# Optimization experiments

Measured on AMD Instinct MI355X. Metric: run time of the kernel, lower is better.

The kernel has to match this reference:

```python
import jax, jax.numpy as jnp
import numpy as np

DIM = 768
HEADS = 12
HEAD_DIM = DIM // HEADS
SCALE = HEAD_DIM ** -0.5
EPS = 1e-6


def setup_inputs() -> dict:
    key = jax.random.key(0)
    ks = jax.random.split(key, 10)
    B, Nq, Nk, C = 4, 4096, 4096, DIM
    std = C ** -0.5
    return {
        "x_q": jax.random.normal(ks[0], (B, Nq, C), jnp.float32),
        "x_kv": jax.random.normal(ks[1], (B, Nk, C), jnp.float32),
        "Wq": jax.random.normal(ks[2], (C, C), jnp.float32) * std,
        "bq": jnp.zeros((C,), jnp.float32),
        "Wk": jax.random.normal(ks[3], (C, C), jnp.float32) * std,
        "bk": jnp.zeros((C,), jnp.float32),
        "Wv": jax.random.normal(ks[4], (C, C), jnp.float32) * std,
        "bv": jnp.zeros((C,), jnp.float32),
        "Wp": jax.random.normal(ks[5], (C, C), jnp.float32) * std,
        "bp": jnp.zeros((C,), jnp.float32),
    }


def _phi(x):
    # ELU(alpha=1) + 1 positive feature map
    return jax.nn.elu(x) + 1.0


def reference(x_q, x_kv, Wq, bq, Wk, bk, Wv, bv, Wp, bp):
    B, Nq, C = x_q.shape
    Nk = x_kv.shape[1]
    h, d = HEADS, HEAD_DIM
    # projections (torch Linear: x @ W.T + b)
    q = x_q @ Wq.T + bq   # [B,Nq,C]
    k = x_kv @ Wk.T + bk  # [B,Nk,C]
    v = x_kv @ Wv.T + bv  # [B,Nk,C]
    # split heads -> [B,h,N,d]
    q = q.reshape(B, Nq, h, d).transpose(0, 2, 1, 3) * SCALE
    k = k.reshape(B, Nk, h, d).transpose(0, 2, 1, 3)
    v = v.reshape(B, Nk, h, d).transpose(0, 2, 1, 3)
    q_phi = _phi(q)
    k_phi = _phi(k)
    # KV state [B,h,d,d] and normalizer sum [B,h,d]
    kv = jnp.einsum('bhnd,bhne->bhde', k_phi, v)
    k_sum = k_phi.sum(axis=2)
    out = jnp.einsum('bhnd,bhde->bhne', q_phi, kv)
    z = jnp.einsum('bhnd,bhd->bhn', q_phi, k_sum)[..., None] + EPS
    out = out / z
    out = out.transpose(0, 2, 1, 3).reshape(B, Nq, C)
    return out @ Wp.T + bp
```

## Files before the change

kernel.cpp:

```cpp
#include <hip/hip_runtime.h>
#include <hip/hip_bf16.h>
#include <cstdint>
#include <cstddef>

#define HD_B   4
#define SEQ    4096
#define CDIM   768
#define HEADS  12
#define HDIM   64
#define MROWS  (HD_B * SEQ)
#define QSCALE 0.125f
#define EPSV   1e-6f

typedef __attribute__((ext_vector_type(8))) short  short8v;
typedef __attribute__((ext_vector_type(4))) float  f32x4;

__device__ __forceinline__ unsigned short f2b(float f) {
    unsigned int u = __float_as_uint(f);
    u += 0x7FFFu + ((u >> 16) & 1u);
    return (unsigned short)(u >> 16);
}
__device__ __forceinline__ float b2f(unsigned short b) {
    return __uint_as_float(((unsigned int)b) << 16);
}
__device__ __forceinline__ float phi_f(float x) {
    return x > 0.f ? x + 1.f : __expf(x);
}

#define GLOAD_LDS16(g, l)                                             \
    __builtin_amdgcn_global_load_lds(                                 \
        (__attribute__((address_space(1))) void*)(void*)(g),          \
        (__attribute__((address_space(3))) void*)(l), 16, 0, 0)

__global__ void wcvt_all(const float* __restrict__ wq, const float* __restrict__ wk,
                         const float* __restrict__ wv, const float* __restrict__ wp,
                         unsigned short* __restrict__ dst) {
    const int y = blockIdx.y;
    const float* src = (y == 0) ? wq : (y == 1) ? wk : (y == 2) ? wv : wp;
    const int i = blockIdx.x * 256 + threadIdx.x;
    float4 v = reinterpret_cast<const float4*>(src)[i];
    ushort4 o;
    o.x = f2b(v.x); o.y = f2b(v.y); o.z = f2b(v.z); o.w = f2b(v.w);
    reinterpret_cast<ushort4*>(dst + (size_t)y * (CDIM * CDIM))[i] = o;
}

template <int KIND>
__global__ __launch_bounds__(256) void gemm_pipe(
    const float* __restrict__ Aq,
    const float* __restrict__ Akv,
    const unsigned short* __restrict__ Abf,
    const unsigned short* __restrict__ Wb,
    const float* __restrict__ b0,
    const float* __restrict__ b1,
    const float* __restrict__ b2,
    unsigned short* __restrict__ out_q,
    unsigned short* __restrict__ out_k,
    unsigned short* __restrict__ out_v,
    float* __restrict__ out_f)
{
    constexpr int K  = CDIM;
    constexpr int NC = (KIND == 0) ? 18 : 6;
    constexpr int T  = NC * 128;
    constexpr int NT = K / 64;

    __shared__ __align__(16) char smem[65536];

    const int tid  = threadIdx.x;
    const int lane = tid & 63;
    const int w    = tid >> 6;
    const int wr   = w >> 1, wc = w & 1;

    const int bid  = blockIdx.x;
    const int s    = (bid & 7) * (T >> 3) + (bid >> 3);
    const int colp = s % NC;
    const int rowp = s / NC;
    const int brow = rowp * 128;
    const int mode = (KIND == 0) ? (colp / 6) : 3;
    const int bcol = (KIND == 0) ? (colp % 6) * 128 : colp * 128;

    const float* A32 = (KIND == 0) ? (mode == 0 ? Aq : Akv) : nullptr;
    const unsigned short* Bp = Wb + ((KIND == 0) ? (size_t)mode * (K * K) : 0);

    const int r8  = lane >> 3;
    const int c8  = ((lane & 7) ^ r8) << 3;
    const int ar  = lane >> 4;
    const int ac  = (lane & 15) << 2;
    const int fr  = lane & 15;
    const int hi4 = lane >> 4;

    f32x4 acc[4][4];
#pragma unroll
    for (int i = 0; i < 4; ++i)
#pragma unroll
        for (int j = 0; j < 4; ++j)
            acc[i][j] = (f32x4){0.f, 0.f, 0.f, 0.f};

    auto stageB = [&](int buf, int k0) {
        char* dst = smem + 32768 + buf * 16384;
#pragma unroll
        for (int g = 0; g < 4; ++g) {
            const unsigned short* src =
                Bp + (size_t)(bcol + w * 32 + g * 8 + r8) * K + k0 + c8;
            GLOAD_LDS16(src, dst + (w * 32 + g * 8) * 128);
        }
    };
    auto stageA16 = [&](int buf, int k0) {
        char* dst = smem + buf * 16384;
#pragma unroll
        for (int g = 0; g < 4; ++g) {
            const unsigned short* src =
                Abf + (size_t)(brow + w * 32 + g * 8 + r8) * K + k0 + c8;
            GLOAD_LDS16(src, dst + (w * 32 + g * 8) * 128);
        }
    };
    auto loadA32 = [&](int k0, float4* f) {
#pragma unroll
        for (int j = 0; j < 8; ++j) {
            const int row = w * 32 + j * 4 + ar;
            f[j] = *(const float4*)(A32 + (size_t)(brow + row) * K + k0 + ac);
        }
    };
    auto writeA32 = [&](int buf, const float4* f) {
        char* dst = smem + buf * 16384;
#pragma unroll
        for (int j = 0; j < 8; ++j) {
            const int row = w * 32 + j * 4 + ar;
            unsigned int p0, p1;
            asm("v_cvt_pk_bf16_f32 %0, %1, %2" : "=v"(p0) : "v"(f[j].x), "v"(f[j].y));
            asm("v_cvt_pk_bf16_f32 %0, %1, %2" : "=v"(p1) : "v"(f[j].z), "v"(f[j].w));
            uint2 pk; pk.x = p0; pk.y = p1;
            *(uint2*)(dst + row * 128 + ((ac << 1) ^ ((row & 7) << 4))) = pk;
        }
    };
    auto compute = [&](int buf) {
        const char* Ab = smem + buf * 16384;
        const char* Bb = smem + 32768 + buf * 16384;
        short8v a[4][2];
#pragma unroll
        for (int i = 0; i < 4; ++i) {
            const int row = wr * 64 + i * 16 + fr;
#pragma unroll
            for (int ks = 0; ks < 2; ++ks)
                a[i][ks] = *(const short8v*)(Ab + row * 128 +
                              ((((ks << 2) + hi4) ^ (row & 7)) << 4));
        }
#pragma unroll
        for (int j = 0; j < 4; ++j) {
            const int row = wc * 64 + j * 16 + fr;
            short8v bb0 = *(const short8v*)(Bb + row * 128 + ((hi4 ^ (row & 7)) << 4));
            short8v bb1 = *(const short8v*)(Bb + row * 128 + (((4 + hi4) ^ (row & 7)) << 4));
#pragma unroll
            for (int i = 0; i < 4; ++i) {
                acc[i][j] = __builtin_amdgcn_mfma_f32_16x16x32_bf16(a[i][0], bb0, acc[i][j], 0, 0, 0);
                acc[i][j] = __builtin_amdgcn_mfma_f32_16x16x32_bf16(a[i][1], bb1, acc[i][j], 0, 0, 0);
            }
        }
    };

    if (KIND == 0) {
        float4 fA[8];
        stageB(0, 0);
        loadA32(0, fA);
        asm volatile("s_waitcnt vmcnt(0)" ::: "memory");
        writeA32(0, fA);
        __syncthreads();
        for (int t = 0; t < NT; ++t) {
            const int cur = t & 1, nxt = cur ^ 1;
            if (t < NT - 1) { stageB(nxt, (t + 1) * 64); loadA32((t + 1) * 64, fA); }
            __builtin_amdgcn_sched_barrier(0);
            compute(cur);
            if (t < NT - 1) {
                asm volatile("s_waitcnt vmcnt(0)" ::: "memory");
                writeA32(nxt, fA);
                __syncthreads();
            }
        }
    } else {
        stageB(0, 0);
        stageA16(0, 0);
        __syncthreads();
        for (int t = 0; t < NT; ++t) {
            const int cur = t & 1, nxt = cur ^ 1;
            if (t < NT - 1) { stageB(nxt, (t + 1) * 64); stageA16(nxt, (t + 1) * 64); }
            __builtin_amdgcn_sched_barrier(0);
            compute(cur);
            if (t < NT - 1) __syncthreads();
        }
    }
    __syncthreads();

    float* ep = (float*)(void*)smem + w * (16 * 68);
    const int rr = lane >> 2;
    const int cb = (lane & 3) * 4;
    const float* bptr = (KIND == 1) ? b0 : (mode == 0 ? b0 : (mode == 1 ? b1 : b2));
    unsigned short* o16 = (KIND == 0)
        ? (mode == 0 ? out_q : (mode == 1 ? out_k : out_v)) : nullptr;

    float4 bb[4];
#pragma unroll
    for (int q = 0; q < 4; ++q)
        bb[q] = *(const float4*)&bptr[bcol + wc * 64 + q * 16 + cb];

#pragma unroll
    for (int i = 0; i < 4; ++i) {
#pragma unroll
        for (int j = 0; j < 4; ++j)
#pragma unroll
            for (int r = 0; r < 4; ++r)
                ep[(hi4 * 4 + r) * 68 + j * 16 + fr] = acc[i][j][r];
#pragma unroll
        for (int q = 0; q < 4; ++q) {
            const int cc = q * 16 + cb;
            f32x4 v = *(const f32x4*)&ep[rr * 68 + cc];
            const int rg = brow + wr * 64 + i * 16 + rr;
            const int cg = bcol + wc * 64 + cc;
            const float4 bq = bb[q];
            if (KIND == 1) {
                float4 ov;
                ov.x = v[0] + bq.x; ov.y = v[1] + bq.y;
                ov.z = v[2] + bq.z; ov.w = v[3] + bq.w;
                *(float4*)(out_f + (size_t)rg * 768 + cg) = ov;
            } else {
                ushort4 ov;
                if (mode == 0) {
                    ov.x = f2b(phi_f((v[0] + bq.x) * QSCALE));
                    ov.y = f2b(phi_f((v[1] + bq.y) * QSCALE));
                    ov.z = f2b(phi_f((v[2] + bq.z) * QSCALE));
                    ov.w = f2b(phi_f((v[3] + bq.w) * QSCALE));
                } else if (mode == 1) {
                    ov.x = f2b(phi_f(v[0] + bq.x));
                    ov.y = f2b(phi_f(v[1] + bq.y));
                    ov.z = f2b(phi_f(v[2] + bq.z));
                    ov.w = f2b(phi_f(v[3] + bq.w));
                } else {
                    ov.x = f2b(v[0] + bq.x);
                    ov.y = f2b(v[1] + bq.y);
                    ov.z = f2b(v[2] + bq.z);
                    ov.w = f2b(v[3] + bq.w);
                }
                *(ushort4*)(o16 + (size_t)rg * 768 + cg) = ov;
            }
        }
    }
}

#define KVCH   128
#define KVITER 2
#define NCHUNK 16

__global__ __launch_bounds__(256) void kv_part(
    const unsigned short* __restrict__ kphi,
    const unsigned short* __restrict__ vmat,
    float* __restrict__ part)
{
    const int bh = blockIdx.y;
    const int b  = bh / HEADS, h = bh % HEADS;
    const int c  = blockIdx.x;
    __shared__ float Kl[KVCH][HDIM];
    __shared__ float Vl[KVCH][HDIM];
    const int t  = threadIdx.x;
    const int i  = t >> 2;
    const int jb = t & 3;

    float acc[16];
#pragma unroll
    for (int jj = 0; jj < 16; ++jj) acc[jj] = 0.f;
    float ksum = 0.f;

    for (int it = 0; it < KVITER; ++it) {
        const size_t rbase = (size_t)b * SEQ + (size_t)c * (KVCH * KVITER) + it * KVCH;
        __syncthreads();
        for (int l = 0; l < KVCH / 32; ++l) {
            int row = l * 32 + (t >> 3);
            int col = (t & 7) << 3;
            const size_t g = (rbase + row) * CDIM + h * HDIM + col;
            int4 kk = *(const int4*)(kphi + g);
            int4 vv = *(const int4*)(vmat + g);
            const unsigned short* kp = (const unsigned short*)&kk;
            const unsigned short* vp = (const unsigned short*)&vv;
#pragma unroll
            for (int q = 0; q < 8; ++q) {
                Kl[row][col + q] = b2f(kp[q]);
                Vl[row][col + q] = b2f(vp[q]);
            }
        }
        __syncthreads();
        for (int n = 0; n < KVCH; ++n) {
            float kf = Kl[n][i];
            const float4* vr = (const float4*)&Vl[n][jb * 16];
            float4 v0 = vr[0], v1 = vr[1], v2 = vr[2], v3 = vr[3];
            acc[0]  += kf * v0.x; acc[1]  += kf * v0.y; acc[2]  += kf * v0.z; acc[3]  += kf * v0.w;
            acc[4]  += kf * v1.x; acc[5]  += kf * v1.y; acc[6]  += kf * v1.z; acc[7]  += kf * v1.w;
            acc[8]  += kf * v2.x; acc[9]  += kf * v2.y; acc[10] += kf * v2.z; acc[11] += kf * v2.w;
            acc[12] += kf * v3.x; acc[13] += kf * v3.y; acc[14] += kf * v3.z; acc[15] += kf * v3.w;
            ksum += kf;
        }
    }
    float* op = part + ((size_t)c * 48 + bh) * 4160;
#pragma unroll
    for (int jj = 0; jj < 16; ++jj) op[i * 64 + jb * 16 + jj] = acc[jj];
    if (jb == 0) op[4096 + i] = ksum;
}

__global__ void kv_finalize(const float* __restrict__ part, float* __restrict__ kv) {
    int idx = blockIdx.x * 256 + threadIdx.x;
    if (idx >= 48 * 4160) return;
    float s = 0.f;
    for (int c = 0; c < NCHUNK; ++c) s += part[(size_t)c * 48 * 4160 + idx];
    kv[idx] = s;
}

__global__ __launch_bounds__(256) void attn_apply(
    const unsigned short* __restrict__ qphi,
    const float* __restrict__ kv,
    unsigned short* __restrict__ attn)
{
    const int h  = blockIdx.y;
    const int m0 = blockIdx.x * 64;
    const int b  = m0 >> 12;
    const int bh = b * HEADS + h;
    __shared__ float kvs[HDIM][HDIM];
    __shared__ float ksums[HDIM];
    __shared__ unsigned short ql[64][HDIM];
    const int t = threadIdx.x;
    const float* kvp = kv + (size_t)bh * 4160;
#pragma unroll
    for (int it = 0; it < 4; ++it) {
        int e = it * 1024 + t * 4;
        *(float4*)&kvs[e >> 6][e & 63] = *(const float4*)&kvp[e];
    }
    if (t < 64) ksums[t] = kvp[4096 + t];
#pragma unroll
    for (int it = 0; it < 2; ++it) {
        int row = it * 32 + (t >> 3);
        int col = (t & 7) << 3;
        *(int4*)&ql[row][col] =
            *(const int4*)(qphi + (size_t)(m0 + row) * CDIM + h * HDIM + col);
    }
    __syncthreads();

    const int r  = t >> 2;
    const int jb = t & 3;
    float acc[16];
#pragma unroll
    for (int jj = 0; jj < 16; ++jj) acc[jj] = 0.f;
    float z = 0.f;
    for (int q8 = 0; q8 < 8; ++q8) {
        short8v qv = *(const short8v*)&ql[r][q8 * 8];
#pragma unroll
        for (int dd = 0; dd < 8; ++dd) {
            float qd = b2f((unsigned short)qv[dd]);
            int d = q8 * 8 + dd;
            const float4* kr = (const float4*)&kvs[d][jb * 16];
            float4 k0 = kr[0], k1 = kr[1], k2 = kr[2], k3 = kr[3];
            acc[0]  += qd * k0.x; acc[1]  += qd * k0.y; acc[2]  += qd * k0.z; acc[3]  += qd * k0.w;
            acc[4]  += qd * k1.x; acc[5]  += qd * k1.y; acc[6]  += qd * k1.z; acc[7]  += qd * k1.w;
            acc[8]  += qd * k2.x; acc[9]  += qd * k2.y; acc[10] += qd * k2.z; acc[11] += qd * k2.w;
            acc[12] += qd * k3.x; acc[13] += qd * k3.y; acc[14] += qd * k3.z; acc[15] += qd * k3.w;
            z += qd * ksums[d];
        }
    }
    const float inv = 1.f / (z + EPSV);
    unsigned short* op = attn + (size_t)(m0 + r) * CDIM + h * HDIM + jb * 16;
#pragma unroll
    for (int jj = 0; jj < 16; ++jj) op[jj] = f2b(acc[jj] * inv);
}

extern "C" void kernel_launch(void* const* d_in, const int* in_sizes, int n_in,
                              void* d_out, int out_size, void* d_ws, size_t ws_size,
                              hipStream_t stream)
{
    const float* x_q  = (const float*)d_in[0];
    const float* x_kv = (const float*)d_in[1];
    const float* Wq   = (const float*)d_in[2];
    const float* bq   = (const float*)d_in[3];
    const float* Wk   = (const float*)d_in[4];
    const float* bk   = (const float*)d_in[5];
    const float* Wv   = (const float*)d_in[6];
    const float* bv   = (const float*)d_in[7];
    const float* Wp   = (const float*)d_in[8];
    const float* bp   = (const float*)d_in[9];
    float* out = (float*)d_out;

    char* ws = (char*)d_ws;
    size_t off = 0;
    auto alloc = [&](size_t bytes) -> char* {
        char* p = ws + off;
        off += (bytes + 255) & ~(size_t)255;
        return p;
    };
    const size_t xbytes = (size_t)MROWS * CDIM * 2;
    const size_t wbytes = (size_t)CDIM * CDIM * 2;
    unsigned short* w16    = (unsigned short*)alloc(4 * wbytes);
    unsigned short* wp16   = w16 + 3 * (CDIM * CDIM);
    unsigned short* qphi   = (unsigned short*)alloc(xbytes);
    unsigned short* kphi   = (unsigned short*)alloc(xbytes);
    unsigned short* v16    = (unsigned short*)alloc(xbytes);
    unsigned short* attn16 = (unsigned short*)alloc(xbytes);
    float* part = (float*)alloc((size_t)NCHUNK * 48 * 4160 * 4);
    float* kvf  = (float*)alloc((size_t)48 * 4160 * 4);

    wcvt_all<<<dim3(576, 4), 256, 0, stream>>>(Wq, Wk, Wv, Wp, w16);

    gemm_pipe<0><<<2304, 256, 0, stream>>>(
        x_q, x_kv, nullptr, w16, bq, bk, bv, qphi, kphi, v16, nullptr);

    kv_part<<<dim3(NCHUNK, 48), 256, 0, stream>>>(kphi, v16, part);
    kv_finalize<<<(48 * 4160 + 255) / 256, 256, 0, stream>>>(part, kvf);
    attn_apply<<<dim3(MROWS / 64, HEADS), 256, 0, stream>>>(qphi, kvf, attn16);

    gemm_pipe<1><<<768, 256, 0, stream>>>(
        nullptr, nullptr, attn16, wp16, bp, nullptr, nullptr,
        nullptr, nullptr, nullptr, out);
}
```

Measured before the change: 224.4 us.

## Pre-convert activations to bf16 and switch GEMM to register-staged single LDS buffer

Adds a combined conversion kernel that turns x_q, x_kv and all four weights into bf16 in one pass, so the QKV GEMM reads bf16 activations instead of converting fp32 inside its main loop. The GEMM drops direct global-to-LDS loads and double buffering. It now prefetches the next tile into registers and writes it to a single 32KB LDS buffer behind two barriers per iteration. This halves LDS use, which may allow more blocks per CU. The cost is an extra full write and read of the bf16 activations through global memory, plus an extra barrier per k-step.

```diff
diff --git a/kernel.cpp b/kernel.cpp
--- a/kernel.cpp
+++ b/kernel.cpp
@@ -27,43 +27,46 @@
     return x > 0.f ? x + 1.f : __expf(x);
 }
 
-#define GLOAD_LDS16(g, l)                                             \
-    __builtin_amdgcn_global_load_lds(                                 \
-        (__attribute__((address_space(1))) void*)(void*)(g),          \
-        (__attribute__((address_space(3))) void*)(l), 16, 0, 0)
-
-__global__ void wcvt_all(const float* __restrict__ wq, const float* __restrict__ wk,
-                         const float* __restrict__ wv, const float* __restrict__ wp,
-                         unsigned short* __restrict__ dst) {
-    const int y = blockIdx.y;
-    const float* src = (y == 0) ? wq : (y == 1) ? wk : (y == 2) ? wv : wp;
+#define N4X 3145728
+#define N4W 147456
+__global__ void cvt_multi(const float* __restrict__ xq, const float* __restrict__ xkv,
+                          const float* __restrict__ wq, const float* __restrict__ wk,
+                          const float* __restrict__ wv, const float* __restrict__ wp,
+                          unsigned short* __restrict__ dst) {
     const int i = blockIdx.x * 256 + threadIdx.x;
-    float4 v = reinterpret_cast<const float4*>(src)[i];
+    const float* src;
+    int off;
+    if (i < N4X)            { src = xq;  off = 0; }
+    else if (i < 2 * N4X)   { src = xkv; off = N4X; }
+    else {
+        const int wi = (i - 2 * N4X) / N4W;
+        src = (wi == 0) ? wq : (wi == 1) ? wk : (wi == 2) ? wv : wp;
+        off = 2 * N4X + wi * N4W;
+    }
+    float4 v = reinterpret_cast<const float4*>(src)[i - off];
     ushort4 o;
     o.x = f2b(v.x); o.y = f2b(v.y); o.z = f2b(v.z); o.w = f2b(v.w);
-    reinterpret_cast<ushort4*>(dst + (size_t)y * (CDIM * CDIM))[i] = o;
+    reinterpret_cast<ushort4*>(dst)[i] = o;
 }
 
 template <int KIND>
-__global__ __launch_bounds__(256) void gemm_pipe(
-    const float* __restrict__ Aq,
-    const float* __restrict__ Akv,
-    const unsigned short* __restrict__ Abf,
+__global__ __launch_bounds__(256) void gemm_t14(
+    const unsigned short* __restrict__ Aq,
+    const unsigned short* __restrict__ Akv,
     const unsigned short* __restrict__ Wb,
-    const float* __restrict__ b0,
-    const float* __restrict__ b1,
+    const float* __restrict__ b0, const float* __restrict__ b1,
     const float* __restrict__ b2,
-    unsigned short* __restrict__ out_q,
-    unsigned short* __restrict__ out_k,
-    unsigned short* __restrict__ out_v,
-    float* __restrict__ out_f)
+    unsigned short* __restrict__ out_q, unsigned short* __restrict__ out_k,
+    unsigned short* __restrict__ out_v, float* __restrict__ out_f)
 {
     constexpr int K  = CDIM;
     constexpr int NC = (KIND == 0) ? 18 : 6;
     constexpr int T  = NC * 128;
     constexpr int NT = K / 64;
 
-    __shared__ __align__(16) char smem[65536];
+    __shared__ __align__(16) char smem[32768];
+    char* As = smem;
+    char* Bs = smem + 16384;
 
     const int tid  = threadIdx.x;
     const int lane = tid & 63;
@@ -78,16 +81,18 @@
     const int mode = (KIND == 0) ? (colp / 6) : 3;
     const int bcol = (KIND == 0) ? (colp % 6) * 128 : colp * 128;
 
-    const float* A32 = (KIND == 0) ? (mode == 0 ? Aq : Akv) : nullptr;
-    const unsigned short* Bp = Wb + ((KIND == 0) ? (size_t)mode * (K * K) : 0);
-
-    const int r8  = lane >> 3;
-    const int c8  = ((lane & 7) ^ r8) << 3;
-    const int ar  = lane >> 4;
-    const int ac  = (lane & 15) << 2;
+    const unsigned short* A16 = (KIND == 0) ? (mode == 0 ? Aq : Akv) : Aq;
+    const unsigned short* Bp  = Wb + ((KIND == 0) ? (size_t)mode * (K * K) : 0);
+
+    const int r8 = lane >> 3;
+    const int c8 = (lane & 7) << 3;
+    const int wbyte = ((lane & 7) ^ r8) << 4;
     const int fr  = lane & 15;
     const int hi4 = lane >> 4;
 
+    const unsigned short* aB = A16 + (size_t)(brow + w * 32 + r8) * K + c8;
+    const unsigned short* bB = Bp  + (size_t)(bcol + w * 32 + r8) * K + c8;
+
     f32x4 acc[4][4];
 #pragma unroll
     for (int i = 0; i < 4; ++i)
@@ -95,60 +100,38 @@
         for (int j = 0; j < 4; ++j)
             acc[i][j] = (f32x4){0.f, 0.f, 0.f, 0.f};
 
-    auto stageB = [&](int buf, int k0) {
-        char* dst = smem + 32768 + buf * 16384;
-#pragma unroll
-        for (int g = 0; g < 4; ++g) {
-            const unsigned short* src =
-                Bp + (size_t)(bcol + w * 32 + g * 8 + r8) * K + k0 + c8;
-            GLOAD_LDS16(src, dst + (w * 32 + g * 8) * 128);
-        }
-    };
-    auto stageA16 = [&](int buf, int k0) {
-        char* dst = smem + buf * 16384;
-#pragma unroll
-        for (int g = 0; g < 4; ++g) {
-            const unsigned short* src =
-                Abf + (size_t)(brow + w * 32 + g * 8 + r8) * K + k0 + c8;
-            GLOAD_LDS16(src, dst + (w * 32 + g * 8) * 128);
-        }
-    };
-    auto loadA32 = [&](int k0, float4* f) {
-#pragma unroll
-        for (int j = 0; j < 8; ++j) {
-            const int row = w * 32 + j * 4 + ar;
-            f[j] = *(const float4*)(A32 + (size_t)(brow + row) * K + k0 + ac);
-        }
-    };
-    auto writeA32 = [&](int buf, const float4* f) {
-        char* dst = smem + buf * 16384;
-#pragma unroll
-        for (int j = 0; j < 8; ++j) {
-            const int row = w * 32 + j * 4 + ar;
-            unsigned int p0, p1;
-            asm("v_cvt_pk_bf16_f32 %0, %1, %2" : "=v"(p0) : "v"(f[j].x), "v"(f[j].y));
-            asm("v_cvt_pk_bf16_f32 %0, %1, %2" : "=v"(p1) : "v"(f[j].z), "v"(f[j].w));
-            uint2 pk; pk.x = p0; pk.y = p1;
-            *(uint2*)(dst + row * 128 + ((ac << 1) ^ ((row & 7) << 4))) = pk;
-        }
-    };
-    auto compute = [&](int buf) {
-        const char* Ab = smem + buf * 16384;
-        const char* Bb = smem + 32768 + buf * 16384;
+    int4 rA[4], rB[4];
+
+#define GLOAD(k0) do {                                                      \
+    _Pragma("unroll")                                                       \
+    for (int g = 0; g < 4; ++g) {                                           \
+        rA[g] = *(const int4*)(aB + (size_t)(g * 8) * K + (k0));            \
+        rB[g] = *(const int4*)(bB + (size_t)(g * 8) * K + (k0));            \
+    } } while (0)
+
+#define SWRITE() do {                                                       \
+    _Pragma("unroll")                                                       \
+    for (int g = 0; g < 4; ++g) {                                           \
+        const int rowl = w * 32 + g * 8 + r8;                               \
+        *(int4*)(As + rowl * 128 + wbyte) = rA[g];                          \
+        *(int4*)(Bs + rowl * 128 + wbyte) = rB[g];                          \
+    } } while (0)
+
+    auto compute = [&]() {
         short8v a[4][2];
 #pragma unroll
         for (int i = 0; i < 4; ++i) {
             const int row = wr * 64 + i * 16 + fr;
 #pragma unroll
             for (int ks = 0; ks < 2; ++ks)
-                a[i][ks] = *(const short8v*)(Ab + row * 128 +
+                a[i][ks] = *(const short8v*)(As + row * 128 +
                               ((((ks << 2) + hi4) ^ (row & 7)) << 4));
         }
 #pragma unroll
         for (int j = 0; j < 4; ++j) {
             const int row = wc * 64 + j * 16 + fr;
-            short8v bb0 = *(const short8v*)(Bb + row * 128 + ((hi4 ^ (row & 7)) << 4));
-            short8v bb1 = *(const short8v*)(Bb + row * 128 + (((4 + hi4) ^ (row & 7)) << 4));
+            short8v bb0 = *(const short8v*)(Bs + row * 128 + ((hi4 ^ (row & 7)) << 4));
+            short8v bb1 = *(const short8v*)(Bs + row * 128 + (((4 + hi4) ^ (row & 7)) << 4));
 #pragma unroll
             for (int i = 0; i < 4; ++i) {
                 acc[i][j] = __builtin_amdgcn_mfma_f32_16x16x32_bf16(a[i][0], bb0, acc[i][j], 0, 0, 0);
@@ -157,37 +140,22 @@
         }
     };
 
-    if (KIND == 0) {
-        float4 fA[8];
-        stageB(0, 0);
-        loadA32(0, fA);
-        asm volatile("s_waitcnt vmcnt(0)" ::: "memory");
-        writeA32(0, fA);
+    GLOAD(0);
+    SWRITE();
+    __syncthreads();
+
+    for (int t = 0; t < NT; ++t) {
+        if (t < NT - 1) GLOAD((t + 1) * 64);
+        __builtin_amdgcn_sched_barrier(0);
+        compute();
         __syncthreads();
-        for (int t = 0; t < NT; ++t) {
-            const int cur = t & 1, nxt = cur ^ 1;
-            if (t < NT - 1) { stageB(nxt, (t + 1) * 64); loadA32((t + 1) * 64, fA); }
-            __builtin_amdgcn_sched_barrier(0);
-            compute(cur);
-            if (t < NT - 1) {
-                asm volatile("s_waitcnt vmcnt(0)" ::: "memory");
-                writeA32(nxt, fA);
-                __syncthreads();
-            }
-        }
-    } else {
-        stageB(0, 0);
-        stageA16(0, 0);
-        __syncthreads();
-        for (int t = 0; t < NT; ++t) {
-            const int cur = t & 1, nxt = cur ^ 1;
-            if (t < NT - 1) { stageB(nxt, (t + 1) * 64); stageA16(nxt, (t + 1) * 64); }
-            __builtin_amdgcn_sched_barrier(0);
-            compute(cur);
-            if (t < NT - 1) __syncthreads();
-        }
-    }
-    __syncthreads();
+        if (t < NT - 1) {
+            SWRITE();
+            __syncthreads();
+        }
+    }
+#undef GLOAD
+#undef SWRITE
 
     float* ep = (float*)(void*)smem + w * (16 * 68);
     const int rr = lane >> 2;
@@ -389,27 +357,32 @@
         off += (bytes + 255) & ~(size_t)255;
         return p;
     };
-    const size_t xbytes = (size_t)MROWS * CDIM * 2;
-    const size_t wbytes = (size_t)CDIM * CDIM * 2;
-    unsigned short* w16    = (unsigned short*)alloc(4 * wbytes);
-    unsigned short* wp16   = w16 + 3 * (CDIM * CDIM);
-    unsigned short* qphi   = (unsigned short*)alloc(xbytes);
-    unsigned short* kphi   = (unsigned short*)alloc(xbytes);
-    unsigned short* v16    = (unsigned short*)alloc(xbytes);
-    unsigned short* attn16 = (unsigned short*)alloc(xbytes);
+    const size_t xelems = (size_t)MROWS * CDIM;
+    const size_t welems = (size_t)CDIM * CDIM;
+
+    unsigned short* cvt16 = (unsigned short*)alloc((2 * xelems + 4 * welems) * 2);
+    unsigned short* xq16  = cvt16;
+    unsigned short* xkv16 = cvt16 + xelems;
+    unsigned short* w16   = cvt16 + 2 * xelems;
+    unsigned short* wp16  = w16 + 3 * welems;
+
+    unsigned short* qphi   = (unsigned short*)alloc(xelems * 2);
+    unsigned short* kphi   = (unsigned short*)alloc(xelems * 2);
+    unsigned short* v16    = (unsigned short*)alloc(xelems * 2);
+    unsigned short* attn16 = (unsigned short*)alloc(xelems * 2);
     float* part = (float*)alloc((size_t)NCHUNK * 48 * 4160 * 4);
     float* kvf  = (float*)alloc((size_t)48 * 4160 * 4);
 
-    wcvt_all<<<dim3(576, 4), 256, 0, stream>>>(Wq, Wk, Wv, Wp, w16);
-
-    gemm_pipe<0><<<2304, 256, 0, stream>>>(
-        x_q, x_kv, nullptr, w16, bq, bk, bv, qphi, kphi, v16, nullptr);
+    cvt_multi<<<26880, 256, 0, stream>>>(x_q, x_kv, Wq, Wk, Wv, Wp, cvt16);
+
+    gemm_t14<0><<<2304, 256, 0, stream>>>(
+        xq16, xkv16, w16, bq, bk, bv, qphi, kphi, v16, nullptr);
 
     kv_part<<<dim3(NCHUNK, 48), 256, 0, stream>>>(kphi, v16, part);
     kv_finalize<<<(48 * 4160 + 255) / 256, 256, 0, stream>>>(part, kvf);
     attn_apply<<<dim3(MROWS / 64, HEADS), 256, 0, stream>>>(qphi, kvf, attn16);
 
-    gemm_pipe<1><<<768, 256, 0, stream>>>(
-        nullptr, nullptr, attn16, wp16, bp, nullptr, nullptr,
+    gemm_t14<1><<<768, 256, 0, stream>>>(
+        attn16, nullptr, wp16, bp, nullptr, nullptr,
         nullptr, nullptr, nullptr, out);
 }
```

Measured after the change: 441.0 us. 1.97x slower.

## Prefetch two K-tiles ahead with counted vmcnt waits in projection GEMMs

Applied to the files above, without the earlier changes.

Restructures both GEMM main loops so that loads for tile t+2 are issued while tile t is computed. Fine-grained s_waitcnt vmcnt(N) counts replace full vmcnt(0) drains, and raw s_barrier replaces __syncthreads. The goal is to keep more global loads in flight and hide memory latency behind MFMA work. In exchange, ordering of LDS reuse now depends on hand-counted outstanding-load values, which is fragile. The trailing sync before the epilogue is also dropped, so the epilogue may write shared memory that other waves are still reading.

```diff
diff --git a/kernel.cpp b/kernel.cpp
--- a/kernel.cpp
+++ b/kernel.cpp
@@ -31,6 +31,15 @@
     __builtin_amdgcn_global_load_lds(                                 \
         (__attribute__((address_space(1))) void*)(void*)(g),          \
         (__attribute__((address_space(3))) void*)(l), 16, 0, 0)
+
+#define VMW12() asm volatile("s_waitcnt vmcnt(12)" ::: "memory")
+#define VMW8()  asm volatile("s_waitcnt vmcnt(8)"  ::: "memory")
+#define VMW4()  asm volatile("s_waitcnt vmcnt(4)"  ::: "memory")
+#define VMW0()  asm volatile("s_waitcnt vmcnt(0)"  ::: "memory")
+#define LGW()   asm volatile("s_waitcnt lgkmcnt(0)" ::: "memory")
+#define SB()    do { __builtin_amdgcn_sched_barrier(0);               \
+                     __builtin_amdgcn_s_barrier();                    \
+                     __builtin_amdgcn_sched_barrier(0); } while (0)
 
 __global__ void wcvt_all(const float* __restrict__ wq, const float* __restrict__ wk,
                          const float* __restrict__ wv, const float* __restrict__ wp,
@@ -45,18 +54,15 @@
 }
 
 template <int KIND>
-__global__ __launch_bounds__(256) void gemm_pipe(
+__global__ __launch_bounds__(256) void gemm_cnt(
     const float* __restrict__ Aq,
     const float* __restrict__ Akv,
     const unsigned short* __restrict__ Abf,
     const unsigned short* __restrict__ Wb,
-    const float* __restrict__ b0,
-    const float* __restrict__ b1,
+    const float* __restrict__ b0, const float* __restrict__ b1,
     const float* __restrict__ b2,
-    unsigned short* __restrict__ out_q,
-    unsigned short* __restrict__ out_k,
-    unsigned short* __restrict__ out_v,
-    float* __restrict__ out_f)
+    unsigned short* __restrict__ out_q, unsigned short* __restrict__ out_k,
+    unsigned short* __restrict__ out_v, float* __restrict__ out_f)
 {
     constexpr int K  = CDIM;
     constexpr int NC = (KIND == 0) ? 18 : 6;
@@ -78,11 +84,11 @@
     const int mode = (KIND == 0) ? (colp / 6) : 3;
     const int bcol = (KIND == 0) ? (colp % 6) * 128 : colp * 128;
 
-    const float* A32 = (KIND == 0) ? (mode == 0 ? Aq : Akv) : nullptr;
-    const unsigned short* Bp = Wb + ((KIND == 0) ? (size_t)mode * (K * K) : 0);
+    const float* A32          = (KIND == 0) ? (mode == 0 ? Aq : Akv) : nullptr;
+    const unsigned short* Bp  = Wb + ((KIND == 0) ? (size_t)mode * (K * K) : 0);
 
     const int r8  = lane >> 3;
-    const int c8  = ((lane & 7) ^ r8) << 3;
+    const int c8e = ((lane & 7) ^ r8) << 3;
     const int ar  = lane >> 4;
     const int ac  = (lane & 15) << 2;
     const int fr  = lane & 15;
@@ -95,39 +101,39 @@
         for (int j = 0; j < 4; ++j)
             acc[i][j] = (f32x4){0.f, 0.f, 0.f, 0.f};
 
-    auto stageB = [&](int buf, int k0) {
+    auto stageB = [&](int buf, int kt) {
         char* dst = smem + 32768 + buf * 16384;
 #pragma unroll
         for (int g = 0; g < 4; ++g) {
             const unsigned short* src =
-                Bp + (size_t)(bcol + w * 32 + g * 8 + r8) * K + k0 + c8;
+                Bp + (size_t)(bcol + w * 32 + g * 8 + r8) * K + kt * 64 + c8e;
             GLOAD_LDS16(src, dst + (w * 32 + g * 8) * 128);
         }
     };
-    auto stageA16 = [&](int buf, int k0) {
+    auto stageA16 = [&](int buf, int kt) {
         char* dst = smem + buf * 16384;
 #pragma unroll
         for (int g = 0; g < 4; ++g) {
             const unsigned short* src =
-                Abf + (size_t)(brow + w * 32 + g * 8 + r8) * K + k0 + c8;
+                Abf + (size_t)(brow + w * 32 + g * 8 + r8) * K + kt * 64 + c8e;
             GLOAD_LDS16(src, dst + (w * 32 + g * 8) * 128);
         }
     };
-    auto loadA32 = [&](int k0, float4* f) {
-#pragma unroll
-        for (int j = 0; j < 8; ++j) {
-            const int row = w * 32 + j * 4 + ar;
-            f[j] = *(const float4*)(A32 + (size_t)(brow + row) * K + k0 + ac);
-        }
-    };
-    auto writeA32 = [&](int buf, const float4* f) {
+    float4 fA[8];
+    auto aload = [&](int kt) {
+#pragma unroll
+        for (int j = 0; j < 8; ++j)
+            fA[j] = *(const float4*)(A32 + (size_t)(brow + w * 32 + j * 4 + ar) * K
+                                     + kt * 64 + ac);
+    };
+    auto awrite = [&](int buf) {
         char* dst = smem + buf * 16384;
 #pragma unroll
         for (int j = 0; j < 8; ++j) {
             const int row = w * 32 + j * 4 + ar;
             unsigned int p0, p1;
-            asm("v_cvt_pk_bf16_f32 %0, %1, %2" : "=v"(p0) : "v"(f[j].x), "v"(f[j].y));
-            asm("v_cvt_pk_bf16_f32 %0, %1, %2" : "=v"(p1) : "v"(f[j].z), "v"(f[j].w));
+            asm("v_cvt_pk_bf16_f32 %0, %1, %2" : "=v"(p0) : "v"(fA[j].x), "v"(fA[j].y));
+            asm("v_cvt_pk_bf16_f32 %0, %1, %2" : "=v"(p1) : "v"(fA[j].z), "v"(fA[j].w));
             uint2 pk; pk.x = p0; pk.y = p1;
             *(uint2*)(dst + row * 128 + ((ac << 1) ^ ((row & 7) << 4))) = pk;
         }
@@ -158,36 +164,39 @@
     };
 
     if (KIND == 0) {
-        float4 fA[8];
+        aload(0);
         stageB(0, 0);
-        loadA32(0, fA);
-        asm volatile("s_waitcnt vmcnt(0)" ::: "memory");
-        writeA32(0, fA);
-        __syncthreads();
+        VMW4();
+        awrite(0);
+        aload(1);
+        stageB(1, 1);
+        LGW();
+        SB();
         for (int t = 0; t < NT; ++t) {
-            const int cur = t & 1, nxt = cur ^ 1;
-            if (t < NT - 1) { stageB(nxt, (t + 1) * 64); loadA32((t + 1) * 64, fA); }
-            __builtin_amdgcn_sched_barrier(0);
-            compute(cur);
+            const int c = t & 1;
+            if (t == NT - 1) { VMW0(); } else { VMW12(); }
+            SB();
+            compute(c);
+            SB();
             if (t < NT - 1) {
-                asm volatile("s_waitcnt vmcnt(0)" ::: "memory");
-                writeA32(nxt, fA);
-                __syncthreads();
+                VMW4();
+                awrite(c ^ 1);
+                if (t < NT - 2) { aload(t + 2); stageB(c, t + 2); }
+                LGW();
             }
         }
     } else {
-        stageB(0, 0);
-        stageA16(0, 0);
-        __syncthreads();
+        stageA16(0, 0); stageB(0, 0);
+        stageA16(1, 1); stageB(1, 1);
         for (int t = 0; t < NT; ++t) {
-            const int cur = t & 1, nxt = cur ^ 1;
-            if (t < NT - 1) { stageB(nxt, (t + 1) * 64); stageA16(nxt, (t + 1) * 64); }
-            __builtin_amdgcn_sched_barrier(0);
-            compute(cur);
-            if (t < NT - 1) __syncthreads();
-        }
-    }
-    __syncthreads();
+            const int c = t & 1;
+            if (t == NT - 1) { VMW0(); } else { VMW8(); }
+            SB();
+            compute(c);
+            SB();
+            if (t < NT - 2) { stageA16(c, t + 2); stageB(c, t + 2); }
+        }
+    }
 
     float* ep = (float*)(void*)smem + w * (16 * 68);
     const int rr = lane >> 2;
@@ -389,27 +398,28 @@
         off += (bytes + 255) & ~(size_t)255;
         return p;
     };
-    const size_t xbytes = (size_t)MROWS * CDIM * 2;
-    const size_t wbytes = (size_t)CDIM * CDIM * 2;
-    unsigned short* w16    = (unsigned short*)alloc(4 * wbytes);
-    unsigned short* wp16   = w16 + 3 * (CDIM * CDIM);
-    unsigned short* qphi   = (unsigned short*)alloc(xbytes);
-    unsigned short* kphi   = (unsigned short*)alloc(xbytes);
-    unsigned short* v16    = (unsigned short*)alloc(xbytes);
-    unsigned short* attn16 = (unsigned short*)alloc(xbytes);
+    const size_t xelems = (size_t)MROWS * CDIM;
+    const size_t welems = (size_t)CDIM * CDIM;
+
+    unsigned short* w16    = (unsigned short*)alloc(4 * welems * 2);
+    unsigned short* wp16   = w16 + 3 * welems;
+    unsigned short* qphi   = (unsigned short*)alloc(xelems * 2);
+    unsigned short* kphi   = (unsigned short*)alloc(xelems * 2);
+    unsigned short* v16    = (unsigned short*)alloc(xelems * 2);
+    unsigned short* attn16 = (unsigned short*)alloc(xelems * 2);
     float* part = (float*)alloc((size_t)NCHUNK * 48 * 4160 * 4);
     float* kvf  = (float*)alloc((size_t)48 * 4160 * 4);
 
     wcvt_all<<<dim3(576, 4), 256, 0, stream>>>(Wq, Wk, Wv, Wp, w16);
 
-    gemm_pipe<0><<<2304, 256, 0, stream>>>(
+    gemm_cnt<0><<<2304, 256, 0, stream>>>(
         x_q, x_kv, nullptr, w16, bq, bk, bv, qphi, kphi, v16, nullptr);
 
     kv_part<<<dim3(NCHUNK, 48), 256, 0, stream>>>(kphi, v16, part);
     kv_finalize<<<(48 * 4160 + 255) / 256, 256, 0, stream>>>(part, kvf);
     attn_apply<<<dim3(MROWS / 64, HEADS), 256, 0, stream>>>(qphi, kvf, attn16);
 
-    gemm_pipe<1><<<768, 256, 0, stream>>>(
+    gemm_cnt<1><<<768, 256, 0, stream>>>(
         nullptr, nullptr, attn16, wp16, bp, nullptr, nullptr,
         nullptr, nullptr, nullptr, out);
 }
```

After: 223.0 us. Within noise of the previous version (-0.6%).
